# Kernel optimization log

Hardware: AMD Instinct MI355X
Metric: run time of the kernel (lower is better)

Reference implementation:

```python
import jax, jax.numpy as jnp
import numpy as np


def setup_inputs() -> dict:
    key = jax.random.key(0)
    k1, k2 = jax.random.split(key)
    B, S, D_IN, D_OUT = 4, 2048, 2048, 8192
    x = jax.random.normal(k1, (B, S, D_IN), dtype=jnp.float32)
    # kaiming_normal_ fan_out, linear: std = 1/sqrt(fan_out)
    weight = jax.random.normal(k2, (D_OUT, D_IN), dtype=jnp.float32) * (1.0 / np.sqrt(D_OUT))
    return {"x": x, "weight": weight}


def reference(x, weight):
    # Per-output-row mean-abs scale, clamped
    scale = jnp.clip(jnp.mean(jnp.abs(weight), axis=1, keepdims=True), 1e-5, None)  # [out, 1]
    w_q = jnp.clip(jnp.round(weight / scale), -1.0, 1.0)  # ternary {-1, 0, 1}
    # STE: value = w_q * scale, gradient flows to weight as identity
    w = weight + jax.lax.stop_gradient(w_q * scale - weight)  # [out, in]
    # F.linear: x @ w.T
    return jnp.einsum('bsi,oi->bso', x, w)
```

## Files before the change

kernel.cpp:

```cpp
#include <hip/hip_runtime.h>
#include <hip/hip_bf16.h>
#include <stdint.h>


typedef float  floatx4 __attribute__((ext_vector_type(4)));
typedef _Float16 f16x8 __attribute__((ext_vector_type(8)));
typedef _Float16 f16x4 __attribute__((ext_vector_type(4)));

#define BM 256
#define BN 256
#define BK 32
#define NSLOT 4

__global__ __launch_bounds__(256) void quant_weight(
    const float* __restrict__ W, f16x4* __restrict__ Q,
    float* __restrict__ scale, int K )
{
    const int wave = threadIdx.x >> 6;
    const int lane = threadIdx.x & 63;
    const int row  = blockIdx.x * 4 + wave;

    const float4* row4 = (const float4*)(W + (size_t)row * K);
    float4 v[8];
    float s = 0.f;
    #pragma unroll
    for (int i = 0; i < 8; ++i) {
        v[i] = row4[lane + 64 * i];
        s += fabsf(v[i].x) + fabsf(v[i].y) + fabsf(v[i].z) + fabsf(v[i].w);
    }
    #pragma unroll
    for (int m = 1; m < 64; m <<= 1) s += __shfl_xor(s, m, 64);

    const float sc  = fmaxf(s / (float)K, 1e-5f);
    if (lane == 0) scale[row] = sc;
    const float inv = 1.0f / sc;

    f16x4* qrow = Q + (size_t)row * (K / 4);
    #pragma unroll
    for (int i = 0; i < 8; ++i) {
        float t[4] = {v[i].x, v[i].y, v[i].z, v[i].w};
        f16x4 o;
        #pragma unroll
        for (int j = 0; j < 4; ++j)
            o[j] = (_Float16)fminf(fmaxf(rintf(t[j] * inv), -1.f), 1.f);
        qrow[lane + 64 * i] = o;
    }
}

__global__ __launch_bounds__(256) void cvt_f16(
    const float4* __restrict__ X, f16x4* __restrict__ Y)
{
    const size_t i = (size_t)blockIdx.x * blockDim.x + threadIdx.x;
    float4 a = X[i];
    f16x4 o;
    o[0] = (_Float16)a.x; o[1] = (_Float16)a.y;
    o[2] = (_Float16)a.z; o[3] = (_Float16)a.w;
    Y[i] = o;
}

__device__ inline void gload_lds16(const void* g, void* l) {
    __builtin_amdgcn_global_load_lds(
        (const __attribute__((address_space(1))) void*)g,
        (__attribute__((address_space(3))) void*)l, 16, 0, 0);
}

__global__ __launch_bounds__(512, 2) void gemm_bt_scaled(
    const _Float16* __restrict__ A,
    const _Float16* __restrict__ B,
    const float* __restrict__ scale,
    float* __restrict__ C,
    int M, int N, int K)
{
    __shared__ __align__(16) _Float16 lds[NSLOT][2][BM * BK];

    const int tid  = threadIdx.x;
    const int lane = tid & 63;
    const int wv   = tid >> 6;
    const int wm   = wv >> 2;
    const int wn   = wv & 3;

    const int nwg = gridDim.x;
    const int cpx = nwg >> 3;
    const int id  = blockIdx.x;
    const int swz = (id & 7) * cpx + (id >> 3);
    const int nbx = N / BN;
    const int by  = swz / nbx;
    const int bx  = swz % nbx;
    const int rowA0 = by * BM;
    const int rowB0 = bx * BN;

    const int lrow  = lane & 15;
    const int kquad = lane >> 4;

    floatx4 acc[8][4] = {};

    int aoff[8], boff[4];
    #pragma unroll
    for (int t = 0; t < 8; ++t) {
        int ra = wm * 128 + t * 16 + lrow;
        aoff[t] = (ra * 4 + (kquad ^ ((ra >> 1) & 3))) * 8;
    }
    #pragma unroll
    for (int t = 0; t < 4; ++t) {
        int rb = wn * 64 + t * 16 + lrow;
        boff[t] = (rb * 4 + (kquad ^ ((rb >> 1) & 3))) * 8;
    }

    const int c0 = tid,        c1 = tid + 512;
    const int r0 = c0 >> 2,    r1 = c1 >> 2;
    const int k0 = (c0 & 3) ^ ((r0 >> 1) & 3);
    const int k1 = (c1 & 3) ^ ((r1 >> 1) & 3);
    const _Float16* pa0 = A + (size_t)(rowA0 + r0) * K + k0 * 8;
    const _Float16* pa1 = A + (size_t)(rowA0 + r1) * K + k1 * 8;
    const _Float16* pb0 = B + (size_t)(rowB0 + r0) * K + k0 * 8;
    const _Float16* pb1 = B + (size_t)(rowB0 + r1) * K + k1 * 8;
    const int eo0 = c0 * 8, eo1 = c1 * 8;

    #pragma unroll
    for (int t = 0; t < 3; ++t) {
        gload_lds16(pa0 + t * BK, &lds[t][0][eo0]);
        gload_lds16(pa1 + t * BK, &lds[t][0][eo1]);
        gload_lds16(pb0 + t * BK, &lds[t][1][eo0]);
        gload_lds16(pb1 + t * BK, &lds[t][1][eo1]);
    }
    pa0 += 3 * BK; pa1 += 3 * BK; pb0 += 3 * BK; pb1 += 3 * BK;

    asm volatile("s_waitcnt vmcnt(8)" ::: "memory");
    __builtin_amdgcn_s_barrier();

    const int NT = K / BK;
    for (int kt0 = 0; kt0 < NT; kt0 += NSLOT) {
        #pragma unroll
        for (int s = 0; s < NSLOT; ++s) {
            const int kt = kt0 + s;
            const bool st = (kt + 3 < NT);
            const int d = (s + 3) & 3;

            f16x8 afr[4], bfr[4];
            #pragma unroll
            for (int t = 0; t < 4; ++t) bfr[t] = *(const f16x8*)&lds[s][1][boff[t]];
            #pragma unroll
            for (int t = 0; t < 4; ++t) afr[t] = *(const f16x8*)&lds[s][0][aoff[t]];
            if (st) {
                gload_lds16(pa0, &lds[d][0][eo0]);
                gload_lds16(pa1, &lds[d][0][eo1]);
            }
            __builtin_amdgcn_s_barrier();
            asm volatile("s_waitcnt lgkmcnt(0)" ::: "memory");
            __builtin_amdgcn_s_setprio(1);
            #pragma unroll
            for (int mt = 0; mt < 4; ++mt)
                #pragma unroll
                for (int nt = 0; nt < 4; ++nt)
                    acc[mt][nt] = __builtin_amdgcn_mfma_f32_16x16x32_f16(
                        afr[mt], bfr[nt], acc[mt][nt], 0, 0, 0);
            __builtin_amdgcn_s_setprio(0);
            __builtin_amdgcn_s_barrier();

            #pragma unroll
            for (int t = 0; t < 4; ++t) afr[t] = *(const f16x8*)&lds[s][0][aoff[t + 4]];
            if (st) {
                gload_lds16(pb0, &lds[d][1][eo0]);
                gload_lds16(pb1, &lds[d][1][eo1]);
                pa0 += BK; pa1 += BK; pb0 += BK; pb1 += BK;
            }
            __builtin_amdgcn_s_barrier();
            asm volatile("s_waitcnt lgkmcnt(0)" ::: "memory");
            __builtin_amdgcn_s_setprio(1);
            #pragma unroll
            for (int mt = 0; mt < 4; ++mt)
                #pragma unroll
                for (int nt = 0; nt < 4; ++nt)
                    acc[mt + 4][nt] = __builtin_amdgcn_mfma_f32_16x16x32_f16(
                        afr[mt], bfr[nt], acc[mt + 4][nt], 0, 0, 0);
            __builtin_amdgcn_s_setprio(0);

            if (kt + 3 < NT) {
                asm volatile("s_waitcnt vmcnt(8)" ::: "memory");
            } else if (kt + 2 < NT) {
                asm volatile("s_waitcnt vmcnt(4)" ::: "memory");
            } else {
                asm volatile("s_waitcnt vmcnt(0)" ::: "memory");
            }
            __builtin_amdgcn_s_barrier();
        }
    }

    const int colb = rowB0 + wn * 64 + lrow;
    const int rowb = rowA0 + wm * 128 + kquad * 4;
    #pragma unroll
    for (int nt = 0; nt < 4; ++nt) {
        const float sc = scale[colb + nt * 16];
        #pragma unroll
        for (int mt = 0; mt < 8; ++mt) {
            #pragma unroll
            for (int r = 0; r < 4; ++r) {
                C[(size_t)(rowb + mt * 16 + r) * N + colb + nt * 16] =
                    acc[mt][nt][r] * sc;
            }
        }
    }
}

extern "C" void kernel_launch(void* const* d_in, const int* in_sizes, int n_in,
                              void* d_out, int out_size, void* d_ws, size_t ws_size,
                              hipStream_t stream) {
    const float* x = (const float*)d_in[0];
    const float* w = (const float*)d_in[1];
    float* out = (float*)d_out;

    const int M = 8192, K = 2048, N = 8192;

    char* ws = (char*)d_ws;
    float*     scale = (float*)ws;
    _Float16*  Xh    = (_Float16*)(ws + 32768);
    _Float16*  Qh    = (_Float16*)(ws + 32768 + (size_t)M * K * 2);

    quant_weight<<<N / 4, 256, 0, stream>>>(w, (f16x4*)Qh, scale, K);
    cvt_f16<<<(M * K / 4) / 256, 256, 0, stream>>>((const float4*)x, (f16x4*)Xh);
    gemm_bt_scaled<<<dim3((M / BM) * (N / BN)), 512, 0, stream>>>(
        Xh, Qh, scale, out, M, N, K);
}
```

Measured before the change: 616.5 us.

## Double-buffer LDS fragments across k-steps and regroup tile raster into row bands

The GEMM main loop now prefetches the next k-slot's A and B register fragments from LDS while the current MFMAs run. It alternates two B fragment register sets and uses partial lgkmcnt waits, so LDS read latency overlaps with matrix math. The global-load wait depth is tightened so the next slot is resident before it is prefetched. The workgroup-to-tile mapping is changed to walk 8-row bands column by column, aiming for better L2 reuse. In exchange it uses more VGPRs and relies on finer-grained wait counts, which risks occupancy loss or subtle hazards.

Result: faster. 597.6 us (-3.1%).

```diff
diff --git a/kernel.cpp b/kernel.cpp
--- a/kernel.cpp
+++ b/kernel.cpp
@@ -82,10 +82,13 @@
     const int nwg = gridDim.x;
     const int cpx = nwg >> 3;
     const int id  = blockIdx.x;
-    const int swz = (id & 7) * cpx + (id >> 3);
+    const int j   = (id >> 3) + (id & 7) * cpx;
     const int nbx = N / BN;
-    const int by  = swz / nbx;
-    const int bx  = swz % nbx;
+    const int per_band = nbx * 8;
+    const int band = j / per_band;
+    const int jj   = j % per_band;
+    const int bx   = jj >> 3;
+    const int by   = band * 8 + (jj & 7);
     const int rowA0 = by * BM;
     const int rowB0 = bx * BN;
 
@@ -125,66 +128,93 @@
     }
     pa0 += 3 * BK; pa1 += 3 * BK; pb0 += 3 * BK; pb1 += 3 * BK;
 
-    asm volatile("s_waitcnt vmcnt(8)" ::: "memory");
+    asm volatile("s_waitcnt vmcnt(4)" ::: "memory");
     __builtin_amdgcn_s_barrier();
 
     const int NT = K / BK;
+
+    f16x8 bfrE[4], bfrO[4], afrA[4], afrB[4];
+
+    #pragma unroll
+    for (int t = 0; t < 4; ++t) bfrE[t] = *(const f16x8*)&lds[0][1][boff[t]];
+    #pragma unroll
+    for (int t = 0; t < 4; ++t) afrA[t] = *(const f16x8*)&lds[0][0][aoff[t]];
+
+#define TILE_STEP(S, BCUR, BNXT)                                             \
+    {                                                                        \
+        const int kt = kt0 + S;                                              \
+        const int d  = (S + 3) & 3;             \
+        const int sn = (S + 1) & 3;                   \
+          \
+        if (kt + 3 < NT) {                                                   \
+            gload_lds16(pa0, &lds[d][0][eo0]);                               \
+            gload_lds16(pa1, &lds[d][0][eo1]);                               \
+        }                                                                    \
+        afrB[0] = *(const f16x8*)&lds[S][0][aoff[4]];                        \
+        afrB[1] = *(const f16x8*)&lds[S][0][aoff[5]];                        \
+        afrB[2] = *(const f16x8*)&lds[S][0][aoff[6]];                        \
+        afrB[3] = *(const f16x8*)&lds[S][0][aoff[7]];                        \
+        __builtin_amdgcn_s_barrier();                                        \
+             \
+        asm volatile("s_waitcnt lgkmcnt(4)" ::: "memory");                   \
+        __builtin_amdgcn_sched_barrier(0);                                   \
+        __builtin_amdgcn_s_setprio(1);                                       \
+        _Pragma("unroll")                                                    \
+        for (int mt = 0; mt < 4; ++mt)                                       \
+            _Pragma("unroll")                                                \
+            for (int nt = 0; nt < 4; ++nt)                                   \
+                acc[mt][nt] = __builtin_amdgcn_mfma_f32_16x16x32_f16(        \
+                    afrA[mt], BCUR[nt], acc[mt][nt], 0, 0, 0);               \
+        __builtin_amdgcn_s_setprio(0);                                       \
+        __builtin_amdgcn_s_barrier();                                        \
+          \
+        if (kt + 3 < NT) {                                                   \
+            gload_lds16(pb0, &lds[d][1][eo0]);                               \
+            gload_lds16(pb1, &lds[d][1][eo1]);                               \
+            pa0 += BK; pa1 += BK; pb0 += BK; pb1 += BK;                      \
+        }                                                                    \
+        if (kt + 1 < NT) {                                                   \
+            BNXT[0] = *(const f16x8*)&lds[sn][1][boff[0]];                   \
+            BNXT[1] = *(const f16x8*)&lds[sn][1][boff[1]];                   \
+            BNXT[2] = *(const f16x8*)&lds[sn][1][boff[2]];                   \
+            BNXT[3] = *(const f16x8*)&lds[sn][1][boff[3]];                   \
+            afrA[0] = *(const f16x8*)&lds[sn][0][aoff[0]];                   \
+            afrA[1] = *(const f16x8*)&lds[sn][0][aoff[1]];                   \
+            afrA[2] = *(const f16x8*)&lds[sn][0][aoff[2]];                   \
+            afrA[3] = *(const f16x8*)&lds[sn][0][aoff[3]];                   \
+        }                                                                    \
+        __builtin_amdgcn_s_barrier();                                        \
+        if (kt + 1 < NT) {                                                   \
+                          \
+            asm volatile("s_waitcnt lgkmcnt(8)" ::: "memory");               \
+        } else {                                                             \
+            asm volatile("s_waitcnt lgkmcnt(0)" ::: "memory");               \
+        }                                                                    \
+        __builtin_amdgcn_sched_barrier(0);                                   \
+        __builtin_amdgcn_s_setprio(1);                                       \
+        _Pragma("unroll")                                                    \
+        for (int mt = 0; mt < 4; ++mt)                                       \
+            _Pragma("unroll")                                                \
+            for (int nt = 0; nt < 4; ++nt)                                   \
+                acc[mt + 4][nt] = __builtin_amdgcn_mfma_f32_16x16x32_f16(    \
+                    afrB[mt], BCUR[nt], acc[mt + 4][nt], 0, 0, 0);           \
+        __builtin_amdgcn_s_setprio(0);                                       \
+                  \
+        if (kt + 4 < NT) {                                                   \
+            asm volatile("s_waitcnt vmcnt(4)" ::: "memory");                 \
+        } else {                                                             \
+            asm volatile("s_waitcnt vmcnt(0)" ::: "memory");                 \
+        }                                                                    \
+        __builtin_amdgcn_s_barrier();                                        \
+    }
+
     for (int kt0 = 0; kt0 < NT; kt0 += NSLOT) {
-        #pragma unroll
-        for (int s = 0; s < NSLOT; ++s) {
-            const int kt = kt0 + s;
-            const bool st = (kt + 3 < NT);
-            const int d = (s + 3) & 3;
-
-            f16x8 afr[4], bfr[4];
-            #pragma unroll
-            for (int t = 0; t < 4; ++t) bfr[t] = *(const f16x8*)&lds[s][1][boff[t]];
-            #pragma unroll
-            for (int t = 0; t < 4; ++t) afr[t] = *(const f16x8*)&lds[s][0][aoff[t]];
-            if (st) {
-                gload_lds16(pa0, &lds[d][0][eo0]);
-                gload_lds16(pa1, &lds[d][0][eo1]);
-            }
-            __builtin_amdgcn_s_barrier();
-            asm volatile("s_waitcnt lgkmcnt(0)" ::: "memory");
-            __builtin_amdgcn_s_setprio(1);
-            #pragma unroll
-            for (int mt = 0; mt < 4; ++mt)
-                #pragma unroll
-                for (int nt = 0; nt < 4; ++nt)
-                    acc[mt][nt] = __builtin_amdgcn_mfma_f32_16x16x32_f16(
-                        afr[mt], bfr[nt], acc[mt][nt], 0, 0, 0);
-            __builtin_amdgcn_s_setprio(0);
-            __builtin_amdgcn_s_barrier();
-
-            #pragma unroll
-            for (int t = 0; t < 4; ++t) afr[t] = *(const f16x8*)&lds[s][0][aoff[t + 4]];
-            if (st) {
-                gload_lds16(pb0, &lds[d][1][eo0]);
-                gload_lds16(pb1, &lds[d][1][eo1]);
-                pa0 += BK; pa1 += BK; pb0 += BK; pb1 += BK;
-            }
-            __builtin_amdgcn_s_barrier();
-            asm volatile("s_waitcnt lgkmcnt(0)" ::: "memory");
-            __builtin_amdgcn_s_setprio(1);
-            #pragma unroll
-            for (int mt = 0; mt < 4; ++mt)
-                #pragma unroll
-                for (int nt = 0; nt < 4; ++nt)
-                    acc[mt + 4][nt] = __builtin_amdgcn_mfma_f32_16x16x32_f16(
-                        afr[mt], bfr[nt], acc[mt + 4][nt], 0, 0, 0);
-            __builtin_amdgcn_s_setprio(0);
-
-            if (kt + 3 < NT) {
-                asm volatile("s_waitcnt vmcnt(8)" ::: "memory");
-            } else if (kt + 2 < NT) {
-                asm volatile("s_waitcnt vmcnt(4)" ::: "memory");
-            } else {
-                asm volatile("s_waitcnt vmcnt(0)" ::: "memory");
-            }
-            __builtin_amdgcn_s_barrier();
-        }
-    }
+        TILE_STEP(0, bfrE, bfrO)
+        TILE_STEP(1, bfrO, bfrE)
+        TILE_STEP(2, bfrE, bfrO)
+        TILE_STEP(3, bfrO, bfrE)
+    }
+#undef TILE_STEP
 
     const int colb = rowB0 + wn * 64 + lrow;
     const int rowb = rowA0 + wm * 128 + kquad * 4;
```
